# Kernel tuning notes

Hardware: AMD Instinct MI355X
Metric: run time of the kernel (lower is better)

Reference implementation:

```python
import jax, jax.numpy as jnp
import numpy as np

NUM_REL = 3


def _inter_layer(h_tail_all, self_tail, self_full, adj, idx, alpha):
    """One InterAgg layer (vectorized over 3 relations' IntraAgg + softmax fusion).
    h_tail_all: [N, d]  last-d features of previous layer for ALL nodes
    self_tail:  [n, d]  same features for the batch nodes
    self_full:  [n, D]  full previous-layer features for the batch nodes
    adj:        [3, N, K] neighbor indices
    idx:        [n]      batch node indices
    alpha:      [2d, 3]  relation attention params
    returns [n, D + 2d]
    """
    W = jax.nn.softmax(alpha, axis=1)  # [2d, 3]
    weighted = jnp.zeros((idx.shape[0], alpha.shape[0]), dtype=h_tail_all.dtype)
    for r in range(NUM_REL):  # fixed small structural loop
        neigh = adj[r][idx]                       # [n, K]
        mean = h_tail_all[neigh].mean(axis=1)     # [n, d]  neighbor-mean (IntraAgg _feats_1)
        intra = jnp.concatenate([mean, self_tail - mean], axis=1)  # [n, 2d]
        weighted = weighted + intra * W[:, r]     # softmax-weighted relation fusion
    return jnp.concatenate([self_full, weighted], axis=1)


def setup_inputs() -> dict:
    key = jax.random.key(0)
    ks = jax.random.split(key, 8)
    N, K, d, B = 50000, 32, 64, 1024
    return {
        "feat_data": jax.random.normal(ks[0], (N, 25), dtype=jnp.float32),
        "W_mlp": jax.random.normal(ks[1], (25, d), dtype=jnp.float32) * 0.2,
        "alpha1": jax.random.normal(ks[2], (2 * d, 3), dtype=jnp.float32) * 0.1,
        "alpha2": jax.random.normal(ks[3], (4 * d, 3), dtype=jnp.float32) * 0.1,
        "linear_w": jax.random.normal(ks[4], (7 * d, 2), dtype=jnp.float32) * 0.05,
        "prior": jax.random.uniform(ks[5], (2,), dtype=jnp.float32, minval=0.01, maxval=1.0),
        "adj": jax.random.randint(ks[6], (3, N, K), 0, N, dtype=jnp.int32),
        "nodes": jax.random.randint(ks[7], (B,), 0, N, dtype=jnp.int32),
    }


def reference(feat_data, W_mlp, alpha1, alpha2, linear_w, prior, adj, nodes):
    N = feat_data.shape[0]
    d = W_mlp.shape[1]
    # MLP layer (layer 0): per-node linear projection
    h0 = feat_data @ W_mlp                                   # [N, d]
    # InterAgg layer 1 over all nodes (so layer 2 can gather neighbor features)
    all_idx = jnp.arange(N)
    h1 = _inter_layer(h0, h0, h0, adj, all_idx, alpha1)      # [N, 3d]
    # InterAgg layer 2 over the batch nodes; uses last 2d cols of layer-1 output
    self_full = h1[nodes]                                    # [B, 3d]
    self_tail = self_full[:, -2 * d:]                        # [B, 2d]
    h2 = _inter_layer(h1[:, -2 * d:], self_tail, self_full, adj, nodes, alpha2)  # [B, 7d]
    # Final linear + log-prior
    return h2 @ linear_w + jnp.log(prior)                    # [B, 2]
```

## Files before the change

kernel.cpp:

```cpp
#include <hip/hip_runtime.h>

typedef unsigned int u32;
typedef unsigned short u16;
typedef _Float16 f16;
typedef __attribute__((ext_vector_type(2))) _Float16 f16x2;
typedef __attribute__((ext_vector_type(4))) _Float16 f16x4;
typedef __attribute__((ext_vector_type(8))) _Float16 f16x8;
typedef __attribute__((ext_vector_type(4))) float f32x4;

#if __has_builtin(__builtin_amdgcn_mfma_f32_16x16x16f16)
#define USE_K16 1
#else
#define USE_K16 0
#endif

__device__ __forceinline__ float bf16_lo(u32 u) { u32 x = u << 16; return __builtin_bit_cast(float, x); }
__device__ __forceinline__ float bf16_hi(u32 u) { u32 x = u & 0xffff0000u; return __builtin_bit_cast(float, x); }
__device__ __forceinline__ float bf16f(u16 v) { u32 x = ((u32)v) << 16; return __builtin_bit_cast(float, x); }
__device__ __forceinline__ u16 f2bf(float f) {
    u32 x = __builtin_bit_cast(u32, f);
    return (u16)((x + 0x7fffu + ((x >> 16) & 1u)) >> 16);
}

__global__ __launch_bounds__(256) void k_prep(const float* __restrict__ feat,
                                              u16* __restrict__ featp, int N) {
    int t = blockIdx.x * 256 + threadIdx.x;
    int row = t >> 5, col = t & 31;
    if (row >= N) return;
    featp[(size_t)row * 32 + col] = (col < 25) ? f2bf(feat[(size_t)row * 25 + col]) : (u16)0;
}

__device__ float m_val(int row, int col, const float* __restrict__ W,
                       const float* __restrict__ a1) {
    if (row >= 84) {
        int k = row - 84;
        return (k < 25 && col >= 64) ? W[k * 64 + (col - 64)] : 0.f;
    }
    int seg = (row >= 56) ? 2 : (row >= 28) ? 1 : 0;
    int k = row - seg * 28;
    if (k >= 25) return 0.f;
    int cc = (col < 64) ? col : col - 64;
    int arow = (col < 64) ? cc : 64 + cc;
    float e0 = __expf(a1[arow * 3 + 0]);
    float e1 = __expf(a1[arow * 3 + 1]);
    float e2 = __expf(a1[arow * 3 + 2]);
    float wt = ((seg == 0) ? e0 : (seg == 1) ? e1 : e2) / (e0 + e1 + e2);
    float v = W[k * 64 + cc] * wt * (1.f / 32.f);
    return (col < 64) ? v : -v;
}

__global__ __launch_bounds__(256) void k_prepM(const float* __restrict__ W,
                                               const float* __restrict__ a1,
                                               f16* __restrict__ Bpack) {
    int idx = blockIdx.x * 256 + threadIdx.x;
#if USE_K16
    int j = idx & 3, l = (idx >> 2) & 63, ks = (idx >> 8) & 7, ct = idx >> 11;
    int row = ks * 16 + ((l >> 4) << 2) + j;
#else
    int j = idx & 7, l = (idx >> 3) & 63, ks = (idx >> 9) & 3, ct = idx >> 11;
    int row = ks * 32 + ((l >> 4) << 3) + j;
#endif
    int col = ct * 16 + (l & 15);
    float v = (row < 112) ? m_val(row, col, W, a1) : 0.f;
    Bpack[idx] = (f16)v;
}

__global__ __launch_bounds__(256) void k_layer1f(const float* __restrict__ feat,
                                                 const u16* __restrict__ featp,
                                                 const int* __restrict__ adj,
                                                 const f16* __restrict__ Bpack,
                                                 u16* __restrict__ w1, int N) {
    __shared__ f16 x[16][136];
    int w = threadIdx.x >> 6;
    int l = threadIdx.x & 63;
    int g = l >> 4;
    int c = l & 15;
    int i0 = blockIdx.x * 16;
    int node = i0 + w * 4 + g;
    int nsafe = (node < N) ? node : 0;

    const u32* fp = (const u32*)featp;
#pragma unroll
    for (int r = 0; r < 3; ++r) {
        const int* arow = adj + ((size_t)r * N + nsafe) * 32;
        int idxA = __builtin_nontemporal_load(arow + c);
        int idxB = __builtin_nontemporal_load(arow + 16 + c);
        float s0 = 0.f, s1 = 0.f;
#pragma unroll
        for (int k = 0; k < 16; ++k) {
            int nb = __shfl(idxA, k, 16);
            u32 u = fp[(size_t)nb * 16 + c];
            s0 += bf16_lo(u);
            s1 += bf16_hi(u);
        }
#pragma unroll
        for (int k = 0; k < 16; ++k) {
            int nb = __shfl(idxB, k, 16);
            u32 u = fp[(size_t)nb * 16 + c];
            s0 += bf16_lo(u);
            s1 += bf16_hi(u);
        }
        if (c < 14) {
            f16x2 o;
            o[0] = (f16)s0;
            o[1] = (f16)s1;
            *(u32*)&x[w * 4 + g][r * 28 + 2 * c] = __builtin_bit_cast(u32, o);
        }
    }
    for (int e = threadIdx.x; e < 16 * 44; e += 256) {
        int row = e / 44, col = 84 + e % 44;
        int nrow = i0 + row;
        float v = (col < 109 && nrow < N) ? feat[(size_t)nrow * 25 + (col - 84)] : 0.f;
        x[row][col] = (f16)v;
    }
    __syncthreads();

#if USE_K16
    f16x4 a[8];
    const f16* xrow = &x[l & 15][(l >> 4) << 2];
#pragma unroll
    for (int ks = 0; ks < 8; ++ks) a[ks] = *(const f16x4*)(xrow + ks * 16);
#pragma unroll
    for (int ctt = 0; ctt < 2; ++ctt) {
        int ct = w * 2 + ctt;
        f32x4 d = {0.f, 0.f, 0.f, 0.f};
        const f16* bp = Bpack + ((size_t)(ct * 8) * 64 + l) * 4;
#pragma unroll
        for (int ks = 0; ks < 8; ++ks) {
            f16x4 b = *(const f16x4*)(bp + ks * 256);
            d = __builtin_amdgcn_mfma_f32_16x16x16f16(a[ks], b, d, 0, 0, 0);
        }
#pragma unroll
        for (int reg = 0; reg < 4; ++reg) {
            int n2 = i0 + ((l >> 4) << 2) + reg;
            if (n2 < N) w1[(size_t)n2 * 128 + ct * 16 + (l & 15)] = f2bf(d[reg]);
        }
    }
#else
    f16x8 a[4];
    const f16* xrow = &x[l & 15][(l >> 4) << 3];
#pragma unroll
    for (int ks = 0; ks < 4; ++ks) a[ks] = *(const f16x8*)(xrow + ks * 32);
#pragma unroll
    for (int ctt = 0; ctt < 2; ++ctt) {
        int ct = w * 2 + ctt;
        f32x4 d = {0.f, 0.f, 0.f, 0.f};
        const f16* bp = Bpack + ((size_t)(ct * 4) * 64 + l) * 8;
#pragma unroll
        for (int ks = 0; ks < 4; ++ks) {
            f16x8 b = *(const f16x8*)(bp + ks * 512);
            d = __builtin_amdgcn_mfma_f32_16x16x32_f16(a[ks], b, d, 0, 0, 0);
        }
#pragma unroll
        for (int reg = 0; reg < 4; ++reg) {
            int n2 = i0 + ((l >> 4) << 2) + reg;
            if (n2 < N) w1[(size_t)n2 * 128 + ct * 16 + (l & 15)] = f2bf(d[reg]);
        }
    }
#endif
}

__global__ __launch_bounds__(128) void k_layer2(const float* __restrict__ feat,
                                                const float* __restrict__ Wmlp,
                                                const u16* __restrict__ w1h,
                                                const float* __restrict__ alpha2,
                                                const float* __restrict__ lw,
                                                const float* __restrict__ prior,
                                                const int* __restrict__ adj,
                                                const int* __restrict__ nodes,
                                                float* __restrict__ out, int N) {
    __shared__ int s_idx[96];
    __shared__ float s_red[4];
    int b = blockIdx.x;
    int i = nodes[b];
    int t = threadIdx.x;

    if (t < 96) {
        int r = t >> 5, k = t & 31;
        s_idx[t] = adj[((size_t)r * N + i) * 32 + k];
    }
    __syncthreads();

    float mean[3];
#pragma unroll
    for (int r = 0; r < 3; ++r) {
        float acc = 0.f;
#pragma unroll
        for (int k = 0; k < 32; ++k)
            acc += bf16f(w1h[(size_t)s_idx[r * 32 + k] * 128 + t]);
        mean[r] = acc * (1.f / 32.f);
    }

    float et[3], eb[3], st = 0.f, sb = 0.f;
#pragma unroll
    for (int r = 0; r < 3; ++r) {
        et[r] = __expf(alpha2[t * 3 + r]);         st += et[r];
        eb[r] = __expf(alpha2[(128 + t) * 3 + r]); sb += eb[r];
    }
    float t2 = 0.f, wb = 0.f;
#pragma unroll
    for (int r = 0; r < 3; ++r) { t2 += et[r] * mean[r]; wb += eb[r] * mean[r]; }
    t2 /= st;
    wb /= sb;

    float t1 = bf16f(w1h[(size_t)i * 128 + t]);
    float t3 = t1 - wb;

    float p0 = t1 * lw[(64 + t) * 2 + 0] + t2 * lw[(192 + t) * 2 + 0] + t3 * lw[(320 + t) * 2 + 0];
    float p1 = t1 * lw[(64 + t) * 2 + 1] + t2 * lw[(192 + t) * 2 + 1] + t3 * lw[(320 + t) * 2 + 1];
    if (t < 64) {
        float t0 = 0.f;
#pragma unroll
        for (int k = 0; k < 25; ++k) t0 += feat[(size_t)i * 25 + k] * Wmlp[k * 64 + t];
        p0 += t0 * lw[t * 2 + 0];
        p1 += t0 * lw[t * 2 + 1];
    }

#pragma unroll
    for (int off = 32; off > 0; off >>= 1) {
        p0 += __shfl_down(p0, off, 64);
        p1 += __shfl_down(p1, off, 64);
    }
    int wv = t >> 6, lane = t & 63;
    if (lane == 0) { s_red[wv * 2 + 0] = p0; s_red[wv * 2 + 1] = p1; }
    __syncthreads();
    if (t == 0) {
        out[b * 2 + 0] = s_red[0] + s_red[2] + __logf(prior[0]);
        out[b * 2 + 1] = s_red[1] + s_red[3] + __logf(prior[1]);
    }
}

extern "C" void kernel_launch(void* const* d_in, const int* in_sizes, int n_in,
                              void* d_out, int out_size, void* d_ws, size_t ws_size,
                              hipStream_t stream) {
    const float* feat   = (const float*)d_in[0];
    const float* Wmlp   = (const float*)d_in[1];
    const float* alpha1 = (const float*)d_in[2];
    const float* alpha2 = (const float*)d_in[3];
    const float* lw     = (const float*)d_in[4];
    const float* prior  = (const float*)d_in[5];
    const int*   adj    = (const int*)d_in[6];
    const int*   nodes  = (const int*)d_in[7];
    float* out = (float*)d_out;

    int N = in_sizes[0] / 25;
    int B = in_sizes[7];

    char* base = (char*)d_ws;
    u16* featp = (u16*)base;
    u16* w1    = (u16*)(base + (size_t)N * 32 * 2);
    f16* Bpack = (f16*)(base + (size_t)N * 32 * 2 + (size_t)N * 128 * 2);

    k_prep   <<<(N * 32 + 255) / 256, 256, 0, stream>>>(feat, featp, N);
    k_prepM  <<<64,                   256, 0, stream>>>(Wmlp, alpha1, Bpack);
    k_layer1f<<<(N + 15) / 16,        256, 0, stream>>>(feat, featp, adj, Bpack, w1, N);
    k_layer2 <<<B,                    128, 0, stream>>>(feat, Wmlp, w1, alpha2, lw, prior, adj, nodes, out, N);
}
```

Measured before the change: 60.34 us.

## Stage adjacency indices in LDS and gather neighbor rows with 16-byte loads

Layer-1 now loads each block's adjacency indices for all three relations into shared memory, so cross-lane shuffles are no longer needed. Each lane fetches a 16-byte chunk of a neighbor's bf16 feature row instead of 4 bytes, and partial sums are reduced across lane quarters with xor shuffles. The shared-memory tile layout moves to 32-column relation segments so the writes line up, and the packed weight matrix rows are remapped to match. This cuts the number of gather instructions, at the cost of extra shared memory and a block barrier.

Result: faster. 55.16 us (-8.6%).

```diff
diff --git a/kernel.cpp b/kernel.cpp
--- a/kernel.cpp
+++ b/kernel.cpp
@@ -7,6 +7,7 @@
 typedef __attribute__((ext_vector_type(4))) _Float16 f16x4;
 typedef __attribute__((ext_vector_type(8))) _Float16 f16x8;
 typedef __attribute__((ext_vector_type(4))) float f32x4;
+typedef __attribute__((ext_vector_type(4))) u32 u32x4;
 
 #if __has_builtin(__builtin_amdgcn_mfma_f32_16x16x16f16)
 #define USE_K16 1
@@ -32,12 +33,12 @@
 
 __device__ float m_val(int row, int col, const float* __restrict__ W,
                        const float* __restrict__ a1) {
-    if (row >= 84) {
-        int k = row - 84;
+    if (row >= 96) {
+        int k = row - 96;
         return (k < 25 && col >= 64) ? W[k * 64 + (col - 64)] : 0.f;
     }
-    int seg = (row >= 56) ? 2 : (row >= 28) ? 1 : 0;
-    int k = row - seg * 28;
+    int seg = row >> 5;
+    int k = row & 31;
     if (k >= 25) return 0.f;
     int cc = (col < 64) ? col : col - 64;
     int arow = (col < 64) ? cc : 64 + cc;
@@ -61,8 +62,7 @@
     int row = ks * 32 + ((l >> 4) << 3) + j;
 #endif
     int col = ct * 16 + (l & 15);
-    float v = (row < 112) ? m_val(row, col, W, a1) : 0.f;
-    Bpack[idx] = (f16)v;
+    Bpack[idx] = (f16)m_val(row, col, W, a1);
 }
 
 __global__ __launch_bounds__(256) void k_layer1f(const float* __restrict__ feat,
@@ -71,47 +71,68 @@
                                                  const f16* __restrict__ Bpack,
                                                  u16* __restrict__ w1, int N) {
     __shared__ f16 x[16][136];
-    int w = threadIdx.x >> 6;
-    int l = threadIdx.x & 63;
-    int g = l >> 4;
-    int c = l & 15;
+    __shared__ int s_idx[16][104];
+    int tid = threadIdx.x;
     int i0 = blockIdx.x * 16;
-    int node = i0 + w * 4 + g;
-    int nsafe = (node < N) ? node : 0;
-
+
+    {
+        int node = tid >> 4, l16 = tid & 15;
+        int nsafe = (i0 + node < N) ? (i0 + node) : 0;
+#pragma unroll
+        for (int j = 0; j < 6; ++j) {
+            int jj = l16 + j * 16;
+            int rr = jj >> 5, kk = jj & 31;
+            s_idx[node][jj] = __builtin_nontemporal_load(adj + ((size_t)rr * N + nsafe) * 32 + kk);
+        }
+    }
+    for (int e2 = tid; e2 < 16 * 40; e2 += 256) {
+        int row = e2 / 40, col = 96 + e2 % 40;
+        int nrow = i0 + row;
+        float v = (col < 121 && nrow < N) ? feat[(size_t)nrow * 25 + (col - 96)] : 0.f;
+        x[row][col] = (f16)v;
+    }
+    __syncthreads();
+
+    int w = tid >> 6;
+    int l = tid & 63;
+    int q = l >> 4;
+    int m = (l >> 2) & 3;
+    int e = l & 3;
+    int nodeLocal = w * 4 + m;
     const u32* fp = (const u32*)featp;
+
 #pragma unroll
     for (int r = 0; r < 3; ++r) {
-        const int* arow = adj + ((size_t)r * N + nsafe) * 32;
-        int idxA = __builtin_nontemporal_load(arow + c);
-        int idxB = __builtin_nontemporal_load(arow + 16 + c);
-        float s0 = 0.f, s1 = 0.f;
-#pragma unroll
-        for (int k = 0; k < 16; ++k) {
-            int nb = __shfl(idxA, k, 16);
-            u32 u = fp[(size_t)nb * 16 + c];
-            s0 += bf16_lo(u);
-            s1 += bf16_hi(u);
-        }
-#pragma unroll
-        for (int k = 0; k < 16; ++k) {
-            int nb = __shfl(idxB, k, 16);
-            u32 u = fp[(size_t)nb * 16 + c];
-            s0 += bf16_lo(u);
-            s1 += bf16_hi(u);
-        }
-        if (c < 14) {
-            f16x2 o;
-            o[0] = (f16)s0;
-            o[1] = (f16)s1;
-            *(u32*)&x[w * 4 + g][r * 28 + 2 * c] = __builtin_bit_cast(u32, o);
-        }
-    }
-    for (int e = threadIdx.x; e < 16 * 44; e += 256) {
-        int row = e / 44, col = 84 + e % 44;
-        int nrow = i0 + row;
-        float v = (col < 109 && nrow < N) ? feat[(size_t)nrow * 25 + (col - 84)] : 0.f;
-        x[row][col] = (f16)v;
+        float acc[8];
+#pragma unroll
+        for (int j = 0; j < 8; ++j) acc[j] = 0.f;
+#pragma unroll
+        for (int k = 0; k < 32; k += 4) {
+            int nb = s_idx[nodeLocal][r * 32 + k + q];
+            u32x4 v = *(const u32x4*)(fp + (size_t)nb * 16 + e * 4);
+            acc[0] += bf16_lo(v[0]); acc[1] += bf16_hi(v[0]);
+            acc[2] += bf16_lo(v[1]); acc[3] += bf16_hi(v[1]);
+            acc[4] += bf16_lo(v[2]); acc[5] += bf16_hi(v[2]);
+            acc[6] += bf16_lo(v[3]); acc[7] += bf16_hi(v[3]);
+        }
+#pragma unroll
+        for (int j = 0; j < 8; ++j) {
+            acc[j] += __shfl_xor(acc[j], 16, 64);
+            acc[j] += __shfl_xor(acc[j], 32, 64);
+        }
+        if (q == 0) {
+            f16x2 p0, p1, p2, p3;
+            p0[0] = (f16)acc[0]; p0[1] = (f16)acc[1];
+            p1[0] = (f16)acc[2]; p1[1] = (f16)acc[3];
+            p2[0] = (f16)acc[4]; p2[1] = (f16)acc[5];
+            p3[0] = (f16)acc[6]; p3[1] = (f16)acc[7];
+            u32x4 ov;
+            ov[0] = __builtin_bit_cast(u32, p0);
+            ov[1] = __builtin_bit_cast(u32, p1);
+            ov[2] = __builtin_bit_cast(u32, p2);
+            ov[3] = __builtin_bit_cast(u32, p3);
+            *(u32x4*)&x[nodeLocal][r * 32 + e * 8] = ov;
+        }
     }
     __syncthreads();
 
```
